# Kernel tuning notes

Hardware: AMD Instinct MI355X
Metric: run time of the kernel (lower is better)

The kernel has to match this reference:

```python
import jax, jax.numpy as jnp
import numpy as np

B, N, D = 8, 2048, 512  # batch, input_dim (tokens), weight_dim


def setup_inputs() -> dict:
    key = jax.random.key(0)
    ks = jax.random.split(key, 7)
    return {
        "query": jax.random.normal(ks[0], (B, N, D), dtype=jnp.float32),
        "key": jax.random.normal(ks[1], (B, N, D), dtype=jnp.float32),
        "value": jax.random.normal(ks[2], (B, N, D), dtype=jnp.float32),
        "W_query": jax.random.normal(ks[3], (D, D), dtype=jnp.float32),
        "W_key": jax.random.normal(ks[4], (D, D), dtype=jnp.float32),
        "W_value": jax.random.normal(ks[5], (D, D), dtype=jnp.float32),
        "self_importance": jnp.zeros((N,), dtype=jnp.float32),
    }


def reference(query, key, value, W_query, W_key, W_value, self_importance):
    d = W_query.shape[0]
    q = jnp.einsum("bnd,de->bne", query, W_query)
    k = jnp.einsum("bnd,de->bne", key, W_key)
    v = jnp.einsum("bnd,de->bne", value, W_value)
    scores = jnp.einsum("bqe,bke->bqk", q, k) / jnp.sqrt(jnp.float32(d))
    # diagonal self-importance bias: eye(N) * clamp(exp(s), max=3)
    importance = jnp.minimum(jnp.exp(self_importance), 3.0)  # [N]
    n = scores.shape[1]
    idx = jnp.arange(n)
    scores = scores.at[:, idx, idx].add(importance)
    attn = jax.nn.softmax(scores, axis=-1)  # [B, N, N]
    entropy_loss = -jnp.mean(jnp.sum(attn * jnp.log(attn + 1e-10), axis=-1))
    out = jnp.einsum("bqk,bke->bqe", attn, v)
    return (out, attn, entropy_loss)
```

## Files before the change

### kernel.cpp

```cpp
#include <hip/hip_runtime.h>
#include <math.h>

#define BB 8
#define NN 2048
#define DD 512

typedef _Float16 halfT;
typedef _Float16 half8 __attribute__((ext_vector_type(8)));
typedef _Float16 half4 __attribute__((ext_vector_type(4)));
typedef float f32x4 __attribute__((ext_vector_type(4)));

#define GLOAD16(gp, sp) __builtin_amdgcn_global_load_lds( \
    (const __attribute__((address_space(1))) void*)(gp), \
    (__attribute__((address_space(3))) void*)(sp), 16, 0, 0)

__global__ __launch_bounds__(256) void wsplit_kernel(
    const float* __restrict__ Wq, const float* __restrict__ Wk, const float* __restrict__ Wv,
    _Float16* __restrict__ qhT, _Float16* __restrict__ qlT,
    _Float16* __restrict__ khT, _Float16* __restrict__ klT,
    _Float16* __restrict__ vhT)
{
    __shared__ float t[64][65];
    const int z = blockIdx.z;
    const float* W = (z == 0) ? Wq : ((z == 1) ? Wk : Wv);
    _Float16* Ph = (z == 0) ? qhT : ((z == 1) ? khT : vhT);
    _Float16* Pl = (z == 0) ? qlT : ((z == 1) ? klT : nullptr);
    const int bx = blockIdx.x * 64, by = blockIdx.y * 64;
    const int tid = threadIdx.x;
    #pragma unroll
    for (int i = 0; i < 16; ++i) {
        const int idx = i * 256 + tid;
        const int r = idx >> 6, c = idx & 63;
        t[r][c] = W[(long)(by + r) * 512 + bx + c];
    }
    __syncthreads();
    #pragma unroll
    for (int i = 0; i < 16; ++i) {
        const int idx = i * 256 + tid;
        const int r = idx >> 6, c = idx & 63;
        const float v = t[c][r];
        const _Float16 h = (_Float16)v;
        const long o = (long)(bx + r) * 512 + by + c;
        Ph[o] = h;
        if (z < 2) Pl[o] = (_Float16)(v - (float)h);
    }
}

__global__ __launch_bounds__(512, 2) void projqk_kernel(
    const float* __restrict__ X0, const float* __restrict__ X1,
    const halfT* __restrict__ B0h, const halfT* __restrict__ B0l,
    const halfT* __restrict__ B1h, const halfT* __restrict__ B1l,
    halfT* __restrict__ O0h, halfT* __restrict__ O0l,
    halfT* __restrict__ O1h, halfT* __restrict__ O1l)
{
    extern __shared__ __align__(16) char smem[];

    const int tid  = threadIdx.x;
    const int lane = tid & 63;
    const int w    = tid >> 6;
    const int wr   = w >> 1, wc = w & 1;

    const int h = blockIdx.x;
    const int L = ((h & 7) << 6) | (h >> 3);
    const int z  = L >> 8;
    const int nx = L & 3, my = (L >> 2) & 63;
    const int bm = my * 256, bn = nx * 128;

    const float* X = z ? X1 : X0;
    const halfT* Bgh = z ? B1h : B0h;
    const halfT* Bgl = z ? B1l : B0l;
    halfT* Oh = z ? O1h : O0h;
    halfT* Ol = z ? O1l : O0l;

    const int b_row   = w * 16 + (lane >> 2);
    const int b_chunk = (lane & 3) ^ ((lane >> 3) & 3);
    const long gB = (long)(bn + b_row) * DD + b_chunk * 8;
    const int ldstB = w * 1024;

    const int a_row0 = tid >> 2;
    const int a_gc   = tid & 3;
    const int a_phys = a_gc ^ ((a_row0 >> 1) & 3);
    const long gA0 = (long)(bm + a_row0) * DD + a_gc * 8;
    const long gA1 = (long)(bm + a_row0 + 128) * DD + a_gc * 8;
    const int aOff0 = a_row0 * 64 + a_phys * 16;
    const int aOff1 = (a_row0 + 128) * 64 + a_phys * 16;

    float ar[16];
    auto loadA = [&](int t) {
        const long kk = (long)t * 32;
        *(float4*)&ar[0]  = *(const float4*)(X + gA0 + kk);
        *(float4*)&ar[4]  = *(const float4*)(X + gA0 + kk + 4);
        *(float4*)&ar[8]  = *(const float4*)(X + gA1 + kk);
        *(float4*)&ar[12] = *(const float4*)(X + gA1 + kk + 4);
    };
    auto stageB = [&](char* buf, int t) {
        const long kk = (long)t * 32;
        GLOAD16(Bgh + gB + kk, buf + 32768 + ldstB);
        GLOAD16(Bgl + gB + kk, buf + 40960 + ldstB);
    };
    auto writeA = [&](char* buf) {
        half8 h0, l0, h1, l1;
        #pragma unroll
        for (int i = 0; i < 8; ++i) {
            const _Float16 hh = (_Float16)ar[i];
            h0[i] = hh; l0[i] = (_Float16)(ar[i] - (float)hh);
        }
        #pragma unroll
        for (int i = 0; i < 8; ++i) {
            const _Float16 hh = (_Float16)ar[8 + i];
            h1[i] = hh; l1[i] = (_Float16)(ar[8 + i] - (float)hh);
        }
        *(half8*)(buf + aOff0)         = h0;
        *(half8*)(buf + 16384 + aOff0) = l0;
        *(half8*)(buf + aOff1)         = h1;
        *(half8*)(buf + 16384 + aOff1) = l1;
    };

    const int lr  = lane & 15;
    const int q16 = lane >> 4;
    const int frag = lr * 64 + ((q16 ^ ((lr >> 1) & 3)) << 4);
    const int abase = wr * 4096 + frag;
    const int bbase = wc * 4096 + frag;

    f32x4 acc[4][4];
    #pragma unroll
    for (int i = 0; i < 4; ++i)
        #pragma unroll
        for (int j = 0; j < 4; ++j) acc[i][j] = (f32x4)0.0f;

    loadA(0);
    stageB(smem, 0);
    writeA(smem);
    asm volatile("s_waitcnt vmcnt(0) lgkmcnt(0)" ::: "memory");
    __builtin_amdgcn_s_barrier();
    __builtin_amdgcn_sched_barrier(0);

    for (int t = 0; t < 16; ++t) {
        char* cur = smem + (size_t)(t & 1) * 49152;
        char* nxt = smem + (size_t)((t + 1) & 1) * 49152;
        const bool pf = (t < 15);

        if (pf) { loadA(t + 1); stageB(nxt, t + 1); }

        half8 ah[4], bh[4], bl[4];
        #pragma unroll
        for (int m = 0; m < 4; ++m)
            ah[m] = *(const half8*)(cur + abase + m * 1024);
        #pragma unroll
        for (int j = 0; j < 4; ++j)
            bh[j] = *(const half8*)(cur + 32768 + bbase + j * 1024);
        __builtin_amdgcn_s_setprio(1);
        #pragma unroll
        for (int m = 0; m < 4; ++m)
            #pragma unroll
            for (int j = 0; j < 4; ++j)
                acc[m][j] = __builtin_amdgcn_mfma_f32_16x16x32_f16(ah[m], bh[j], acc[m][j], 0, 0, 0);
        __builtin_amdgcn_s_setprio(0);

        #pragma unroll
        for (int j = 0; j < 4; ++j)
            bl[j] = *(const half8*)(cur + 40960 + bbase + j * 1024);
        __builtin_amdgcn_s_setprio(1);
        #pragma unroll
        for (int m = 0; m < 4; ++m)
            #pragma unroll
            for (int j = 0; j < 4; ++j)
                acc[m][j] = __builtin_amdgcn_mfma_f32_16x16x32_f16(ah[m], bl[j], acc[m][j], 0, 0, 0);
        __builtin_amdgcn_s_setprio(0);

        __builtin_amdgcn_s_setprio(1);
        #pragma unroll
        for (int m = 0; m < 4; ++m) {
            const half8 al = *(const half8*)(cur + 16384 + abase + m * 1024);
            #pragma unroll
            for (int j = 0; j < 4; ++j)
                acc[m][j] = __builtin_amdgcn_mfma_f32_16x16x32_f16(al, bh[j], acc[m][j], 0, 0, 0);
        }
        __builtin_amdgcn_s_setprio(0);

        if (pf) writeA(nxt);
        asm volatile("s_waitcnt vmcnt(0) lgkmcnt(0)" ::: "memory");
        __builtin_amdgcn_s_barrier();
        __builtin_amdgcn_sched_barrier(0);
    }

    #pragma unroll
    for (int m = 0; m < 4; ++m) {
        const int rb = bm + wr * 64 + m * 16 + (q16 << 2);
        #pragma unroll
        for (int j = 0; j < 4; ++j) {
            const int gc = bn + wc * 64 + j * 16 + lr;
            #pragma unroll
            for (int r = 0; r < 4; ++r) {
                const float vv = acc[m][j][r];
                const _Float16 hh = (_Float16)vv;
                const long o = (long)(rb + r) * DD + gc;
                Oh[o] = hh;
                Ol[o] = (_Float16)(vv - (float)hh);
            }
        }
    }
}

__global__ __launch_bounds__(256) void vproj_kernel(
    const float* __restrict__ Af, const _Float16* __restrict__ Bgh,
    _Float16* __restrict__ Oh)
{
    __shared__ __align__(16) _Float16 smem[2 * 128 * 32];
    _Float16* Ah = smem;
    _Float16* Bh = smem + 4096;

    const int tid  = threadIdx.x;
    const int lane = tid & 63;
    const int w    = tid >> 6;
    const int wr   = w >> 1, wc = w & 1;
    const int bm   = blockIdx.y * 128, bn = blockIdx.x * 128;

    f32x4 acc[4][4];
    #pragma unroll
    for (int i = 0; i < 4; ++i)
        #pragma unroll
        for (int j = 0; j < 4; ++j) acc[i][j] = (f32x4)0.0f;

    for (int k0 = 0; k0 < DD; k0 += 32) {
        #pragma unroll
        for (int i = 0; i < 2; ++i) {
            const int c   = i * 256 + w * 64 + lane;
            const int row = c >> 2, sl = c & 3;
            const long g  = (long)(bn + row) * DD + k0 + sl * 8;
            const int lb  = (i * 256 + w * 64) * 8;
            GLOAD16(Bgh + g, Bh + lb);
        }
        #pragma unroll
        for (int i = 0; i < 4; ++i) {
            const int c = tid + i * 256;
            const int row = c >> 3, q4 = c & 7;
            const float4 v = *(const float4*)(Af + (long)(bm + row) * DD + k0 + q4 * 4);
            half4 h;
            h[0] = (_Float16)v.x; h[1] = (_Float16)v.y;
            h[2] = (_Float16)v.z; h[3] = (_Float16)v.w;
            *(half4*)&Ah[row * 32 + q4 * 4] = h;
        }
        __syncthreads();

        half8 ah[4], bh[4];
        #pragma unroll
        for (int f = 0; f < 4; ++f) {
            const int arr = wr * 64 + f * 16 + (lane & 15);
            ah[f] = *(const half8*)&Ah[arr * 32 + ((lane >> 4) << 3)];
            const int brr = wc * 64 + f * 16 + (lane & 15);
            bh[f] = *(const half8*)&Bh[brr * 32 + ((lane >> 4) << 3)];
        }
        #pragma unroll
        for (int i = 0; i < 4; ++i)
            #pragma unroll
            for (int j = 0; j < 4; ++j)
                acc[i][j] = __builtin_amdgcn_mfma_f32_16x16x32_f16(ah[i], bh[j], acc[i][j], 0, 0, 0);
        __syncthreads();
    }

    #pragma unroll
    for (int i = 0; i < 4; ++i) {
        const int rb = bm + wr * 64 + i * 16 + ((lane >> 4) << 2);
        #pragma unroll
        for (int j = 0; j < 4; ++j) {
            const int gc = bn + wc * 64 + j * 16 + (lane & 15);
            half4 hv;
            #pragma unroll
            for (int r = 0; r < 4; ++r) hv[r] = (_Float16)acc[i][j][r];
            const int b = rb >> 11, rIn = rb & 2047;
            *(half4*)&Oh[((long)b * 512 + gc) * 2048 + rIn] = hv;
        }
    }
}

__global__ __launch_bounds__(512, 2) void scores256_kernel(
    const halfT* __restrict__ qh, const halfT* __restrict__ ql,
    const halfT* __restrict__ kh, const halfT* __restrict__ kl,
    float* __restrict__ C, const float* __restrict__ si, float scale)
{
    extern __shared__ __align__(16) char smem[];

    const int tid  = threadIdx.x;
    const int lane = tid & 63;
    const int w    = tid >> 6;
    const int wr   = w >> 2, wc = w & 3;

    int flat = (blockIdx.z << 6) | (blockIdx.y << 3) | blockIdx.x;
    flat = ((flat & 7) << 6) | (flat >> 3);
    const int bx = flat & 7, by = (flat >> 3) & 7, bz = flat >> 6;
    const int bm = by * 256, bn = bx * 256;

    const long zoff = (long)bz * NN * DD;
    const halfT* A_h = qh + zoff;
    const halfT* A_l = ql + zoff;
    const halfT* B_h = kh + zoff;
    const halfT* B_l = kl + zoff;

    const int s_row   = w * 16 + (lane >> 2);
    const int s_chunk = (lane & 3) ^ ((lane >> 3) & 3);
    const long gA = (long)(bm + s_row) * DD + s_chunk * 8;
    const long gB = (long)(bn + s_row) * DD + s_chunk * 8;
    const int ldst = w * 1024;
    const long rstep = (long)128 * DD;

    auto stage = [&](char* buf, int t) {
        const long kk = (long)t * 32;
        GLOAD16(A_h + gA + kk,         buf + ldst);
        GLOAD16(A_h + gA + rstep + kk, buf + 8192 + ldst);
        GLOAD16(A_l + gA + kk,         buf + 16384 + ldst);
        GLOAD16(A_l + gA + rstep + kk, buf + 16384 + 8192 + ldst);
        GLOAD16(B_h + gB + kk,         buf + 32768 + ldst);
        GLOAD16(B_h + gB + rstep + kk, buf + 32768 + 8192 + ldst);
        GLOAD16(B_l + gB + kk,         buf + 49152 + ldst);
        GLOAD16(B_l + gB + rstep + kk, buf + 49152 + 8192 + ldst);
    };

    const int lr   = lane & 15;
    const int q16  = lane >> 4;
    const int fswz = (lr >> 1) & 3;
    const int frag = lr * 64 + ((q16 ^ fswz) << 4);
    const int abase = wr * 8192 + frag;
    const int bbase = wc * 4096 + frag;

    f32x4 acc[8][4];
    #pragma unroll
    for (int m = 0; m < 8; ++m)
        #pragma unroll
        for (int n = 0; n < 4; ++n) acc[m][n] = (f32x4)0.0f;

    stage(smem, 0);
    asm volatile("s_waitcnt vmcnt(0)" ::: "memory");
    __builtin_amdgcn_s_barrier();

    for (int t = 0; t < 16; ++t) {
        char* cur = smem + (size_t)(t & 1) * 65536;
        char* nxt = smem + (size_t)((t + 1) & 1) * 65536;

        if (t < 15) stage(nxt, t + 1);

        half8 ah[8], bh[4], bl[4];
        #pragma unroll
        for (int n = 0; n < 4; ++n)
            bh[n] = *(const half8*)(cur + 32768 + bbase + n * 1024);
        #pragma unroll
        for (int m = 0; m < 8; ++m)
            ah[m] = *(const half8*)(cur + abase + m * 1024);
        __builtin_amdgcn_s_setprio(1);
        #pragma unroll
        for (int m = 0; m < 8; ++m)
            #pragma unroll
            for (int n = 0; n < 4; ++n)
                acc[m][n] = __builtin_amdgcn_mfma_f32_16x16x32_f16(ah[m], bh[n], acc[m][n], 0, 0, 0);
        __builtin_amdgcn_s_setprio(0);

        #pragma unroll
        for (int n = 0; n < 4; ++n)
            bl[n] = *(const half8*)(cur + 49152 + bbase + n * 1024);
        __builtin_amdgcn_s_setprio(1);
        #pragma unroll
        for (int m = 0; m < 8; ++m)
            #pragma unroll
            for (int n = 0; n < 4; ++n)
                acc[m][n] = __builtin_amdgcn_mfma_f32_16x16x32_f16(ah[m], bl[n], acc[m][n], 0, 0, 0);
        __builtin_amdgcn_s_setprio(0);

        __builtin_amdgcn_s_setprio(1);
        #pragma unroll
        for (int m = 0; m < 8; ++m) {
            const half8 al = *(const half8*)(cur + 16384 + abase + m * 1024);
            #pragma unroll
            for (int n = 0; n < 4; ++n)
                acc[m][n] = __builtin_amdgcn_mfma_f32_16x16x32_f16(al, bh[n], acc[m][n], 0, 0, 0);
        }
        __builtin_amdgcn_s_setprio(0);

        if (t < 15) {
            asm volatile("s_waitcnt vmcnt(0)" ::: "memory");
            __builtin_amdgcn_s_barrier();
        }
    }

    float* Cz = C + (long)bz * NN * NN;
    #pragma unroll
    for (int m = 0; m < 8; ++m) {
        const int rb = bm + wr * 128 + m * 16 + ((lane >> 4) << 2);
        #pragma unroll
        for (int n = 0; n < 4; ++n) {
            const int gc = bn + wc * 64 + n * 16 + (lane & 15);
            #pragma unroll
            for (int r = 0; r < 4; ++r) {
                const int gr = rb + r;
                float vv = acc[m][n][r] * scale;
                if (gr == gc) vv += fminf(expf(si[gr]), 3.0f);
                Cz[(long)gr * NN + gc] = vv;
            }
        }
    }
}

__global__ __launch_bounds__(512, 2) void av_kernel(
    const halfT* __restrict__ P, const halfT* __restrict__ V,
    float* __restrict__ O)
{
    extern __shared__ __align__(16) char smem[];

    const int tid  = threadIdx.x;
    const int lane = tid & 63;
    const int w    = tid >> 6;
    const int wr   = w >> 1, wc = w & 1;

    int flat = blockIdx.x;
    flat = ((flat & 7) << 5) | (flat >> 3);
    const int nx = flat & 3, my = (flat >> 2) & 7, bz = flat >> 5;
    const int bm = my * 256, bn = nx * 128;

    const halfT* A = P + (long)bz * NN * NN;
    const halfT* B = V + (long)bz * DD * NN;

    const int s_row   = w * 16 + (lane >> 2);
    const int s_chunk = (lane & 3) ^ ((lane >> 3) & 3);
    const long gA = (long)(bm + s_row) * NN + s_chunk * 8;
    const long gB = (long)(bn + s_row) * NN + s_chunk * 8;
    const int ldst = w * 1024;
    const long rstep = (long)128 * NN;

    auto stage = [&](char* buf, int t) {
        const long kk = (long)t * 32;
        GLOAD16(A + gA + kk,         buf + ldst);
        GLOAD16(A + gA + rstep + kk, buf + 8192 + ldst);
        GLOAD16(B + gB + kk,         buf + 16384 + ldst);
    };

    const int lr  = lane & 15;
    const int q16 = lane >> 4;
    const int frag = lr * 64 + ((q16 ^ ((lr >> 1) & 3)) << 4);
    const int abase = wr * 4096 + frag;
    const int bbase = wc * 4096 + frag;

    f32x4 acc[4][4];
    #pragma unroll
    for (int m = 0; m < 4; ++m)
        #pragma unroll
        for (int j = 0; j < 4; ++j) acc[m][j] = (f32x4)0.0f;

    stage(smem, 0);
    asm volatile("s_waitcnt vmcnt(0)" ::: "memory");
    __builtin_amdgcn_s_barrier();
    __builtin_amdgcn_sched_barrier(0);

    for (int t = 0; t < 64; ++t) {
        char* cur = smem + (size_t)(t & 1) * 24576;
        char* nxt = smem + (size_t)((t + 1) & 1) * 24576;

        if (t < 63) stage(nxt, t + 1);

        half8 ah[4], bh[4];
        #pragma unroll
        for (int m = 0; m < 4; ++m)
            ah[m] = *(const half8*)(cur + abase + m * 1024);
        #pragma unroll
        for (int j = 0; j < 4; ++j)
            bh[j] = *(const half8*)(cur + 16384 + bbase + j * 1024);
        __builtin_amdgcn_s_setprio(1);
        #pragma unroll
        for (int m = 0; m < 4; ++m)
            #pragma unroll
            for (int j = 0; j < 4; ++j)
                acc[m][j] = __builtin_amdgcn_mfma_f32_16x16x32_f16(ah[m], bh[j], acc[m][j], 0, 0, 0);
        __builtin_amdgcn_s_setprio(0);

        if (t < 63) {
            asm volatile("s_waitcnt vmcnt(0)" ::: "memory");
            __builtin_amdgcn_s_barrier();
        }
    }

    float* Oz = O + (long)bz * NN * DD;
    #pragma unroll
    for (int m = 0; m < 4; ++m) {
        const int rb = bm + wr * 64 + m * 16 + (q16 << 2);
        #pragma unroll
        for (int j = 0; j < 4; ++j) {
            const int gc = bn + wc * 64 + j * 16 + lr;
            #pragma unroll
            for (int r = 0; r < 4; ++r)
                Oz[(long)(rb + r) * DD + gc] = acc[m][j][r];
        }
    }
}

__global__ __launch_bounds__(256) void softmax_entropy_kernel(
    float* __restrict__ attn, _Float16* __restrict__ ah, float* __restrict__ partials)
{
    __shared__ float red[4];
    const long row = blockIdx.x;
    float* p = attn + row * (long)NN;
    _Float16* ph = ah + row * (long)NN;
    const int tid = threadIdx.x;
    const int base = tid * 8;

    float4 va = *(const float4*)(p + base);
    float4 vb = *(const float4*)(p + base + 4);
    float v[8] = {va.x, va.y, va.z, va.w, vb.x, vb.y, vb.z, vb.w};

    float m = v[0];
    #pragma unroll
    for (int i = 1; i < 8; ++i) m = fmaxf(m, v[i]);
    #pragma unroll
    for (int o = 32; o; o >>= 1) m = fmaxf(m, __shfl_xor(m, o, 64));
    if ((tid & 63) == 0) red[tid >> 6] = m;
    __syncthreads();
    m = fmaxf(fmaxf(red[0], red[1]), fmaxf(red[2], red[3]));

    float t[8];
    float s = 0.f;
    #pragma unroll
    for (int i = 0; i < 8; ++i) { t[i] = v[i] - m; v[i] = expf(t[i]); s += v[i]; }
    #pragma unroll
    for (int o = 32; o; o >>= 1) s += __shfl_xor(s, o, 64);
    __syncthreads();
    if ((tid & 63) == 0) red[tid >> 6] = s;
    __syncthreads();
    s = red[0] + red[1] + red[2] + red[3];

    const float inv = 1.0f / s;
    const float lns = logf(s);
    float e = 0.f;
    float pv[8];
    #pragma unroll
    for (int i = 0; i < 8; ++i) {
        pv[i] = v[i] * inv;
        e = fmaf(pv[i], t[i] - lns, e);
    }
    *(float4*)(p + base)     = make_float4(pv[0], pv[1], pv[2], pv[3]);
    *(float4*)(p + base + 4) = make_float4(pv[4], pv[5], pv[6], pv[7]);
    half8 h;
    #pragma unroll
    for (int i = 0; i < 8; ++i) h[i] = (_Float16)pv[i];
    *(half8*)(ph + base) = h;

    #pragma unroll
    for (int o = 32; o; o >>= 1) e += __shfl_xor(e, o, 64);
    __syncthreads();
    if ((tid & 63) == 0) red[tid >> 6] = e;
    __syncthreads();
    if (tid == 0) partials[row] = red[0] + red[1] + red[2] + red[3];
}

__global__ __launch_bounds__(256) void ent_reduce_kernel(
    const float* __restrict__ partials, float* __restrict__ ent)
{
    __shared__ float red[4];
    float s = 0.f;
    for (int i = threadIdx.x; i < BB * NN; i += 256) s += partials[i];
    #pragma unroll
    for (int o = 32; o; o >>= 1) s += __shfl_xor(s, o, 64);
    if ((threadIdx.x & 63) == 0) red[threadIdx.x >> 6] = s;
    __syncthreads();
    if (threadIdx.x == 0)
        *ent = -(red[0] + red[1] + red[2] + red[3]) / (float)(BB * NN);
}

extern "C" void kernel_launch(void* const* d_in, const int* in_sizes, int n_in,
                              void* d_out, int out_size, void* d_ws, size_t ws_size,
                              hipStream_t stream) {
    const float* query = (const float*)d_in[0];
    const float* key   = (const float*)d_in[1];
    const float* value = (const float*)d_in[2];
    const float* Wq    = (const float*)d_in[3];
    const float* Wk    = (const float*)d_in[4];
    const float* Wv    = (const float*)d_in[5];
    const float* si    = (const float*)d_in[6];

    float* out  = (float*)d_out;
    float* attn = out + (size_t)BB * NN * DD;
    float* ent  = attn + (size_t)BB * NN * NN;

    const size_t NK = (size_t)BB * NN * DD;
    _Float16* ws16 = (_Float16*)d_ws;
    _Float16* qh = ws16;
    _Float16* ql = qh + NK;
    _Float16* kh = ql + NK;
    _Float16* kl = kh + NK;
    _Float16* vT = kl + NK;
    _Float16* WqhT = vT + NK;
    _Float16* WqlT = WqhT + DD * DD;
    _Float16* WkhT = WqlT + DD * DD;
    _Float16* WklT = WkhT + DD * DD;
    _Float16* WvhT = WklT + DD * DD;
    float* partials = (float*)(WvhT + DD * DD);
    _Float16* attn_h = ws16;

    const dim3 blk(256);
    const float inv_sqrt_d = 0.044194173824159216f;

    wsplit_kernel<<<dim3(8, 8, 3), blk, 0, stream>>>(Wq, Wk, Wv,
        WqhT, WqlT, WkhT, WklT, WvhT);

    projqk_kernel<<<dim3(512), dim3(512), 98304, stream>>>(
        query, key, WqhT, WqlT, WkhT, WklT, qh, ql, kh, kl);
    vproj_kernel<<<dim3(4, 128, 1), blk, 0, stream>>>(value, WvhT, vT);

    scores256_kernel<<<dim3(8, 8, 8), dim3(512), 131072, stream>>>(
        qh, ql, kh, kl, attn, si, inv_sqrt_d);

    softmax_entropy_kernel<<<dim3(BB * NN), blk, 0, stream>>>(attn, attn_h, partials);
    ent_reduce_kernel<<<dim3(1), blk, 0, stream>>>(partials, ent);

    av_kernel<<<dim3(256), dim3(512), 49152, stream>>>(attn_h, vT, out);
}
```

Baseline: 314.4 us.

## Triple-buffer scores and AV GEMMs; shrink scores tile to 256x128

Both the scores GEMM and the AV GEMM move from double to triple buffering in LDS. The next-next stage is prefetched and the wait is a partial vmcnt, so global loads stay in flight across one extra iteration. The scores kernel's block tile also shrinks from 256x256 to 256x128, which cuts per-wave accumulators and doubles the grid. In exchange the kernels use more LDS per block (scores 144KB, AV 72KB), which may limit occupancy, and the smaller tile loses some A-tile reuse.

```diff
diff --git a/kernel.cpp b/kernel.cpp
--- a/kernel.cpp
+++ b/kernel.cpp
@@ -284,12 +284,12 @@
     const int tid  = threadIdx.x;
     const int lane = tid & 63;
     const int w    = tid >> 6;
-    const int wr   = w >> 2, wc = w & 3;
-
-    int flat = (blockIdx.z << 6) | (blockIdx.y << 3) | blockIdx.x;
-    flat = ((flat & 7) << 6) | (flat >> 3);
-    const int bx = flat & 7, by = (flat >> 3) & 7, bz = flat >> 6;
-    const int bm = by * 256, bn = bx * 256;
+    const int wr   = w >> 1, wc = w & 1;
+
+    int flat = (blockIdx.z << 7) | (blockIdx.y << 4) | blockIdx.x;
+    flat = ((flat & 7) << 7) | (flat >> 3);
+    const int bx = flat & 15, by = (flat >> 4) & 7, bz = flat >> 7;
+    const int bm = by * 256, bn = bx * 128;
 
     const long zoff = (long)bz * NN * DD;
     const halfT* A_h = qh + zoff;
@@ -311,44 +311,43 @@
         GLOAD16(A_l + gA + kk,         buf + 16384 + ldst);
         GLOAD16(A_l + gA + rstep + kk, buf + 16384 + 8192 + ldst);
         GLOAD16(B_h + gB + kk,         buf + 32768 + ldst);
-        GLOAD16(B_h + gB + rstep + kk, buf + 32768 + 8192 + ldst);
-        GLOAD16(B_l + gB + kk,         buf + 49152 + ldst);
-        GLOAD16(B_l + gB + rstep + kk, buf + 49152 + 8192 + ldst);
+        GLOAD16(B_l + gB + kk,         buf + 40960 + ldst);
     };
 
-    const int lr   = lane & 15;
-    const int q16  = lane >> 4;
-    const int fswz = (lr >> 1) & 3;
-    const int frag = lr * 64 + ((q16 ^ fswz) << 4);
-    const int abase = wr * 8192 + frag;
+    const int lr  = lane & 15;
+    const int q16 = lane >> 4;
+    const int frag = lr * 64 + ((q16 ^ ((lr >> 1) & 3)) << 4);
+    const int abase = wr * 4096 + frag;
     const int bbase = wc * 4096 + frag;
 
-    f32x4 acc[8][4];
-    #pragma unroll
-    for (int m = 0; m < 8; ++m)
+    f32x4 acc[4][4];
+    #pragma unroll
+    for (int m = 0; m < 4; ++m)
         #pragma unroll
         for (int n = 0; n < 4; ++n) acc[m][n] = (f32x4)0.0f;
 
     stage(smem, 0);
-    asm volatile("s_waitcnt vmcnt(0)" ::: "memory");
+    stage(smem + 49152, 1);
+    asm volatile("s_waitcnt vmcnt(6)" ::: "memory");
     __builtin_amdgcn_s_barrier();
-
+    __builtin_amdgcn_sched_barrier(0);
+
+    int cb = 0;
     for (int t = 0; t < 16; ++t) {
-        char* cur = smem + (size_t)(t & 1) * 65536;
-        char* nxt = smem + (size_t)((t + 1) & 1) * 65536;
-
-        if (t < 15) stage(nxt, t + 1);
-
-        half8 ah[8], bh[4], bl[4];
+        char* cur = smem + (size_t)cb * 49152;
+        const int nb = (cb + 2 == 3) ? 0 : ((cb + 2 == 4) ? 1 : cb + 2);
+        if (t < 14) stage(smem + (size_t)nb * 49152, t + 2);
+
+        half8 ah[4], bh[4], bl[4];
         #pragma unroll
         for (int n = 0; n < 4; ++n)
             bh[n] = *(const half8*)(cur + 32768 + bbase + n * 1024);
         #pragma unroll
-        for (int m = 0; m < 8; ++m)
+        for (int m = 0; m < 4; ++m)
             ah[m] = *(const half8*)(cur + abase + m * 1024);
         __builtin_amdgcn_s_setprio(1);
         #pragma unroll
-        for (int m = 0; m < 8; ++m)
+        for (int m = 0; m < 4; ++m)
             #pragma unroll
             for (int n = 0; n < 4; ++n)
                 acc[m][n] = __builtin_amdgcn_mfma_f32_16x16x32_f16(ah[m], bh[n], acc[m][n], 0, 0, 0);
@@ -356,10 +355,10 @@
 
         #pragma unroll
         for (int n = 0; n < 4; ++n)
-            bl[n] = *(const half8*)(cur + 49152 + bbase + n * 1024);
+            bl[n] = *(const half8*)(cur + 40960 + bbase + n * 1024);
         __builtin_amdgcn_s_setprio(1);
         #pragma unroll
-        for (int m = 0; m < 8; ++m)
+        for (int m = 0; m < 4; ++m)
             #pragma unroll
             for (int n = 0; n < 4; ++n)
                 acc[m][n] = __builtin_amdgcn_mfma_f32_16x16x32_f16(ah[m], bl[n], acc[m][n], 0, 0, 0);
@@ -367,7 +366,7 @@
 
         __builtin_amdgcn_s_setprio(1);
         #pragma unroll
-        for (int m = 0; m < 8; ++m) {
+        for (int m = 0; m < 4; ++m) {
             const half8 al = *(const half8*)(cur + 16384 + abase + m * 1024);
             #pragma unroll
             for (int n = 0; n < 4; ++n)
@@ -376,18 +375,21 @@
         __builtin_amdgcn_s_setprio(0);
 
         if (t < 15) {
-            asm volatile("s_waitcnt vmcnt(0)" ::: "memory");
+            if (t < 14) { asm volatile("s_waitcnt vmcnt(6)" ::: "memory"); }
+            else        { asm volatile("s_waitcnt vmcnt(0)" ::: "memory"); }
             __builtin_amdgcn_s_barrier();
-        }
+            __builtin_amdgcn_sched_barrier(0);
+        }
+        cb = (cb + 1 == 3) ? 0 : cb + 1;
     }
 
     float* Cz = C + (long)bz * NN * NN;
     #pragma unroll
-    for (int m = 0; m < 8; ++m) {
-        const int rb = bm + wr * 128 + m * 16 + ((lane >> 4) << 2);
+    for (int m = 0; m < 4; ++m) {
+        const int rb = bm + wr * 64 + m * 16 + (q16 << 2);
         #pragma unroll
         for (int n = 0; n < 4; ++n) {
-            const int gc = bn + wc * 64 + n * 16 + (lane & 15);
+            const int gc = bn + wc * 64 + n * 16 + lr;
             #pragma unroll
             for (int r = 0; r < 4; ++r) {
                 const int gr = rb + r;
@@ -445,15 +447,16 @@
         for (int j = 0; j < 4; ++j) acc[m][j] = (f32x4)0.0f;
 
     stage(smem, 0);
-    asm volatile("s_waitcnt vmcnt(0)" ::: "memory");
+    stage(smem + 24576, 1);
+    asm volatile("s_waitcnt vmcnt(3)" ::: "memory");
     __builtin_amdgcn_s_barrier();
     __builtin_amdgcn_sched_barrier(0);
 
+    int cb = 0;
     for (int t = 0; t < 64; ++t) {
-        char* cur = smem + (size_t)(t & 1) * 24576;
-        char* nxt = smem + (size_t)((t + 1) & 1) * 24576;
-
-        if (t < 63) stage(nxt, t + 1);
+        char* cur = smem + (size_t)cb * 24576;
+        const int nb = (cb + 2 == 3) ? 0 : ((cb + 2 == 4) ? 1 : cb + 2);
+        if (t < 62) stage(smem + (size_t)nb * 24576, t + 2);
 
         half8 ah[4], bh[4];
         #pragma unroll
@@ -471,9 +474,12 @@
         __builtin_amdgcn_s_setprio(0);
 
         if (t < 63) {
-            asm volatile("s_waitcnt vmcnt(0)" ::: "memory");
+            if (t < 62) { asm volatile("s_waitcnt vmcnt(3)" ::: "memory"); }
+            else        { asm volatile("s_waitcnt vmcnt(0)" ::: "memory"); }
             __builtin_amdgcn_s_barrier();
-        }
+            __builtin_amdgcn_sched_barrier(0);
+        }
+        cb = (cb + 1 == 3) ? 0 : cb + 1;
     }
 
     float* Oz = O + (long)bz * NN * DD;
@@ -602,11 +608,11 @@
         query, key, WqhT, WqlT, WkhT, WklT, qh, ql, kh, kl);
     vproj_kernel<<<dim3(4, 128, 1), blk, 0, stream>>>(value, WvhT, vT);
 
-    scores256_kernel<<<dim3(8, 8, 8), dim3(512), 131072, stream>>>(
+    scores256_kernel<<<dim3(16, 8, 8), dim3(512), 147456, stream>>>(
         qh, ql, kh, kl, attn, si, inv_sqrt_d);
 
     softmax_entropy_kernel<<<dim3(BB * NN), blk, 0, stream>>>(attn, attn_h, partials);
     ent_reduce_kernel<<<dim3(1), blk, 0, stream>>>(partials, ent);
 
-    av_kernel<<<dim3(256), dim3(512), 49152, stream>>>(attn_h, vT, out);
-}
+    av_kernel<<<dim3(256), dim3(512), 73728, stream>>>(attn_h, vT, out);
+}
```

New measurement: 315.6 us. Within noise of the previous version (+0.4%).

## Fold V projection into fused proj kernel and triple-buffer the AV GEMM

Applied to the files above, without the earlier changes.

Removes the separate V-projection kernel. Its tiles now run as extra blocks of the Q/K projection kernel in a single-precision (high-part only) mode with the transposed fp16 output, so all three projections share one launch and fill the GPU together. The AV kernel changes from double- to triple-buffered LDS staging with a prefetch distance of two and partial vmcnt waits, raising shared memory per block to hide global-load latency. The cost is more LDS per block in av_kernel, which may lower occupancy, plus a few runtime branches on the projection mode.

```diff
diff --git a/kernel.cpp b/kernel.cpp
--- a/kernel.cpp
+++ b/kernel.cpp
@@ -46,12 +46,14 @@
     }
 }
 
-__global__ __launch_bounds__(512, 2) void projqk_kernel(
-    const float* __restrict__ X0, const float* __restrict__ X1,
+__global__ __launch_bounds__(512, 2) void proj_kernel(
+    const float* __restrict__ X0, const float* __restrict__ X1, const float* __restrict__ X2,
     const halfT* __restrict__ B0h, const halfT* __restrict__ B0l,
     const halfT* __restrict__ B1h, const halfT* __restrict__ B1l,
+    const halfT* __restrict__ B2h,
     halfT* __restrict__ O0h, halfT* __restrict__ O0l,
-    halfT* __restrict__ O1h, halfT* __restrict__ O1l)
+    halfT* __restrict__ O1h, halfT* __restrict__ O1l,
+    halfT* __restrict__ O2)
 {
     extern __shared__ __align__(16) char smem[];
 
@@ -61,16 +63,23 @@
     const int wr   = w >> 1, wc = w & 1;
 
     const int h = blockIdx.x;
-    const int L = ((h & 7) << 6) | (h >> 3);
-    const int z  = L >> 8;
-    const int nx = L & 3, my = (L >> 2) & 63;
+    int z, nx, my;
+    if (h < 512) {
+        const int L = ((h & 7) << 6) | (h >> 3);
+        z = L >> 8; nx = L & 3; my = (L >> 2) & 63;
+    } else {
+        const int hv = h - 512;
+        const int L = ((hv & 7) << 5) | (hv >> 3);
+        z = 2; nx = L & 3; my = L >> 2;
+    }
     const int bm = my * 256, bn = nx * 128;
-
-    const float* X = z ? X1 : X0;
-    const halfT* Bgh = z ? B1h : B0h;
-    const halfT* Bgl = z ? B1l : B0l;
-    halfT* Oh = z ? O1h : O0h;
-    halfT* Ol = z ? O1l : O0l;
+    const bool full = (z < 2);
+
+    const float* X = (z == 0) ? X0 : ((z == 1) ? X1 : X2);
+    const halfT* Bgh = (z == 0) ? B0h : ((z == 1) ? B1h : B2h);
+    const halfT* Bgl = (z == 0) ? B0l : B1l;
+    halfT* Oh = (z == 0) ? O0h : O1h;
+    halfT* Ol = (z == 0) ? O0l : O1l;
 
     const int b_row   = w * 16 + (lane >> 2);
     const int b_chunk = (lane & 3) ^ ((lane >> 3) & 3);
@@ -96,7 +105,7 @@
     auto stageB = [&](char* buf, int t) {
         const long kk = (long)t * 32;
         GLOAD16(Bgh + gB + kk, buf + 32768 + ldstB);
-        GLOAD16(Bgl + gB + kk, buf + 40960 + ldstB);
+        if (full) GLOAD16(Bgl + gB + kk, buf + 40960 + ldstB);
     };
     auto writeA = [&](char* buf) {
         half8 h0, l0, h1, l1;
@@ -110,10 +119,12 @@
             const _Float16 hh = (_Float16)ar[8 + i];
             h1[i] = hh; l1[i] = (_Float16)(ar[8 + i] - (float)hh);
         }
-        *(half8*)(buf + aOff0)         = h0;
-        *(half8*)(buf + 16384 + aOff0) = l0;
-        *(half8*)(buf + aOff1)         = h1;
-        *(half8*)(buf + 16384 + aOff1) = l1;
+        *(half8*)(buf + aOff0) = h0;
+        *(half8*)(buf + aOff1) = h1;
+        if (full) {
+            *(half8*)(buf + 16384 + aOff0) = l0;
+            *(half8*)(buf + 16384 + aOff1) = l1;
+        }
     };
 
     const int lr  = lane & 15;
@@ -157,26 +168,28 @@
                 acc[m][j] = __builtin_amdgcn_mfma_f32_16x16x32_f16(ah[m], bh[j], acc[m][j], 0, 0, 0);
         __builtin_amdgcn_s_setprio(0);
 
-        #pragma unroll
-        for (int j = 0; j < 4; ++j)
-            bl[j] = *(const half8*)(cur + 40960 + bbase + j * 1024);
-        __builtin_amdgcn_s_setprio(1);
-        #pragma unroll
-        for (int m = 0; m < 4; ++m)
+        if (full) {
             #pragma unroll
             for (int j = 0; j < 4; ++j)
-                acc[m][j] = __builtin_amdgcn_mfma_f32_16x16x32_f16(ah[m], bl[j], acc[m][j], 0, 0, 0);
-        __builtin_amdgcn_s_setprio(0);
-
-        __builtin_amdgcn_s_setprio(1);
-        #pragma unroll
-        for (int m = 0; m < 4; ++m) {
-            const half8 al = *(const half8*)(cur + 16384 + abase + m * 1024);
-            #pragma unroll
-            for (int j = 0; j < 4; ++j)
-                acc[m][j] = __builtin_amdgcn_mfma_f32_16x16x32_f16(al, bh[j], acc[m][j], 0, 0, 0);
-        }
-        __builtin_amdgcn_s_setprio(0);
+                bl[j] = *(const half8*)(cur + 40960 + bbase + j * 1024);
+            __builtin_amdgcn_s_setprio(1);
+            #pragma unroll
+            for (int m = 0; m < 4; ++m)
+                #pragma unroll
+                for (int j = 0; j < 4; ++j)
+                    acc[m][j] = __builtin_amdgcn_mfma_f32_16x16x32_f16(ah[m], bl[j], acc[m][j], 0, 0, 0);
+            __builtin_amdgcn_s_setprio(0);
+
+            __builtin_amdgcn_s_setprio(1);
+            #pragma unroll
+            for (int m = 0; m < 4; ++m) {
+                const half8 al = *(const half8*)(cur + 16384 + abase + m * 1024);
+                #pragma unroll
+                for (int j = 0; j < 4; ++j)
+                    acc[m][j] = __builtin_amdgcn_mfma_f32_16x16x32_f16(al, bh[j], acc[m][j], 0, 0, 0);
+            }
+            __builtin_amdgcn_s_setprio(0);
+        }
 
         if (pf) writeA(nxt);
         asm volatile("s_waitcnt vmcnt(0) lgkmcnt(0)" ::: "memory");
@@ -184,92 +197,36 @@
         __builtin_amdgcn_sched_barrier(0);
     }
 
-    #pragma unroll
-    for (int m = 0; m < 4; ++m) {
-        const int rb = bm + wr * 64 + m * 16 + (q16 << 2);
-        #pragma unroll
-        for (int j = 0; j < 4; ++j) {
-            const int gc = bn + wc * 64 + j * 16 + lr;
-            #pragma unroll
-            for (int r = 0; r < 4; ++r) {
-                const float vv = acc[m][j][r];
-                const _Float16 hh = (_Float16)vv;
-                const long o = (long)(rb + r) * DD + gc;
-                Oh[o] = hh;
-                Ol[o] = (_Float16)(vv - (float)hh);
+    if (full) {
+        #pragma unroll
+        for (int m = 0; m < 4; ++m) {
+            const int rb = bm + wr * 64 + m * 16 + (q16 << 2);
+            #pragma unroll
+            for (int j = 0; j < 4; ++j) {
+                const int gc = bn + wc * 64 + j * 16 + lr;
+                #pragma unroll
+                for (int r = 0; r < 4; ++r) {
+                    const float vv = acc[m][j][r];
+                    const _Float16 hh = (_Float16)vv;
+                    const long o = (long)(rb + r) * DD + gc;
+                    Oh[o] = hh;
+                    Ol[o] = (_Float16)(vv - (float)hh);
+                }
             }
         }
-    }
-}
-
-__global__ __launch_bounds__(256) void vproj_kernel(
-    const float* __restrict__ Af, const _Float16* __restrict__ Bgh,
-    _Float16* __restrict__ Oh)
-{
-    __shared__ __align__(16) _Float16 smem[2 * 128 * 32];
-    _Float16* Ah = smem;
-    _Float16* Bh = smem + 4096;
-
-    const int tid  = threadIdx.x;
-    const int lane = tid & 63;
-    const int w    = tid >> 6;
-    const int wr   = w >> 1, wc = w & 1;
-    const int bm   = blockIdx.y * 128, bn = blockIdx.x * 128;
-
-    f32x4 acc[4][4];
-    #pragma unroll
-    for (int i = 0; i < 4; ++i)
-        #pragma unroll
-        for (int j = 0; j < 4; ++j) acc[i][j] = (f32x4)0.0f;
-
-    for (int k0 = 0; k0 < DD; k0 += 32) {
-        #pragma unroll
-        for (int i = 0; i < 2; ++i) {
-            const int c   = i * 256 + w * 64 + lane;
-            const int row = c >> 2, sl = c & 3;
-            const long g  = (long)(bn + row) * DD + k0 + sl * 8;
-            const int lb  = (i * 256 + w * 64) * 8;
-            GLOAD16(Bgh + g, Bh + lb);
-        }
-        #pragma unroll
-        for (int i = 0; i < 4; ++i) {
-            const int c = tid + i * 256;
-            const int row = c >> 3, q4 = c & 7;
-            const float4 v = *(const float4*)(Af + (long)(bm + row) * DD + k0 + q4 * 4);
-            half4 h;
-            h[0] = (_Float16)v.x; h[1] = (_Float16)v.y;
-            h[2] = (_Float16)v.z; h[3] = (_Float16)v.w;
-            *(half4*)&Ah[row * 32 + q4 * 4] = h;
-        }
-        __syncthreads();
-
-        half8 ah[4], bh[4];
-        #pragma unroll
-        for (int f = 0; f < 4; ++f) {
-            const int arr = wr * 64 + f * 16 + (lane & 15);
-            ah[f] = *(const half8*)&Ah[arr * 32 + ((lane >> 4) << 3)];
-            const int brr = wc * 64 + f * 16 + (lane & 15);
-            bh[f] = *(const half8*)&Bh[brr * 32 + ((lane >> 4) << 3)];
-        }
-        #pragma unroll
-        for (int i = 0; i < 4; ++i)
-            #pragma unroll
-            for (int j = 0; j < 4; ++j)
-                acc[i][j] = __builtin_amdgcn_mfma_f32_16x16x32_f16(ah[i], bh[j], acc[i][j], 0, 0, 0);
-        __syncthreads();
-    }
-
-    #pragma unroll
-    for (int i = 0; i < 4; ++i) {
-        const int rb = bm + wr * 64 + i * 16 + ((lane >> 4) << 2);
-        #pragma unroll
-        for (int j = 0; j < 4; ++j) {
-            const int gc = bn + wc * 64 + j * 16 + (lane & 15);
-            half4 hv;
-            #pragma unroll
-            for (int r = 0; r < 4; ++r) hv[r] = (_Float16)acc[i][j][r];
-            const int b = rb >> 11, rIn = rb & 2047;
-            *(half4*)&Oh[((long)b * 512 + gc) * 2048 + rIn] = hv;
+    } else {
+        #pragma unroll
+        for (int m = 0; m < 4; ++m) {
+            const int rb = bm + wr * 64 + m * 16 + (q16 << 2);
+            #pragma unroll
+            for (int j = 0; j < 4; ++j) {
+                const int gc = bn + wc * 64 + j * 16 + lr;
+                half4 hv;
+                #pragma unroll
+                for (int r = 0; r < 4; ++r) hv[r] = (_Float16)acc[m][j][r];
+                const int b = rb >> 11, rIn = rb & 2047;
+                *(half4*)&O2[((long)b * 512 + gc) * 2048 + rIn] = hv;
+            }
         }
     }
 }
@@ -445,15 +402,16 @@
         for (int j = 0; j < 4; ++j) acc[m][j] = (f32x4)0.0f;
 
     stage(smem, 0);
-    asm volatile("s_waitcnt vmcnt(0)" ::: "memory");
+    stage(smem + 24576, 1);
+    asm volatile("s_waitcnt vmcnt(3)" ::: "memory");
     __builtin_amdgcn_s_barrier();
     __builtin_amdgcn_sched_barrier(0);
 
+    int cb = 0;
     for (int t = 0; t < 64; ++t) {
-        char* cur = smem + (size_t)(t & 1) * 24576;
-        char* nxt = smem + (size_t)((t + 1) & 1) * 24576;
-
-        if (t < 63) stage(nxt, t + 1);
+        char* cur = smem + (size_t)cb * 24576;
+        const int nb = (cb + 2 >= 3) ? cb - 1 : cb + 2;
+        if (t < 62) stage(smem + (size_t)nb * 24576, t + 2);
 
         half8 ah[4], bh[4];
         #pragma unroll
@@ -471,9 +429,12 @@
         __builtin_amdgcn_s_setprio(0);
 
         if (t < 63) {
-            asm volatile("s_waitcnt vmcnt(0)" ::: "memory");
+            if (t < 62) { asm volatile("s_waitcnt vmcnt(3)" ::: "memory"); }
+            else        { asm volatile("s_waitcnt vmcnt(0)" ::: "memory"); }
             __builtin_amdgcn_s_barrier();
-        }
+            __builtin_amdgcn_sched_barrier(0);
+        }
+        cb = (cb + 1 == 3) ? 0 : cb + 1;
     }
 
     float* Oz = O + (long)bz * NN * DD;
@@ -598,9 +559,9 @@
     wsplit_kernel<<<dim3(8, 8, 3), blk, 0, stream>>>(Wq, Wk, Wv,
         WqhT, WqlT, WkhT, WklT, WvhT);
 
-    projqk_kernel<<<dim3(512), dim3(512), 98304, stream>>>(
-        query, key, WqhT, WqlT, WkhT, WklT, qh, ql, kh, kl);
-    vproj_kernel<<<dim3(4, 128, 1), blk, 0, stream>>>(value, WvhT, vT);
+    proj_kernel<<<dim3(768), dim3(512), 98304, stream>>>(
+        query, key, value, WqhT, WqlT, WkhT, WklT, WvhT,
+        qh, ql, kh, kl, vT);
 
     scores256_kernel<<<dim3(8, 8, 8), dim3(512), 131072, stream>>>(
         qh, ql, kh, kl, attn, si, inv_sqrt_d);
@@ -608,5 +569,5 @@
     softmax_entropy_kernel<<<dim3(BB * NN), blk, 0, stream>>>(attn, attn_h, partials);
     ent_reduce_kernel<<<dim3(1), blk, 0, stream>>>(partials, ent);
 
-    av_kernel<<<dim3(256), dim3(512), 49152, stream>>>(attn_h, vT, out);
-}
+    av_kernel<<<dim3(256), dim3(512), 73728, stream>>>(attn_h, vT, out);
+}
```

After: 293.5 us, median of 4. -6.6%, faster.
